# Kernel tuning notes

Hardware: AMD Instinct MI355X
Metric: run time of the kernel (lower is better)

The kernel has to match this reference:

```python
import jax, jax.numpy as jnp
import numpy as np

CHANNELS, STYLE_DIM, N_HEADS, N_TOK = 512, 256, 2, 50
HEAD_DIM = STYLE_DIM // N_HEADS
SCALE = STYLE_DIM ** (-0.5)


def setup_inputs() -> dict:
    key = jax.random.key(0)
    ks = jax.random.split(key, 12)
    B, T = 16, 4096
    s = lambda fan_in: 1.0 / np.sqrt(fan_in)
    return {
        "x": jax.random.normal(ks[0], (B, CHANNELS, T), jnp.float32),
        "style": jax.random.normal(ks[1], (B, N_TOK, STYLE_DIM), jnp.float32),
        "key_emb": jax.random.normal(ks[2], (1, N_TOK, STYLE_DIM), jnp.float32) * 0.3,
        "Wq": jax.random.uniform(ks[3], (STYLE_DIM, CHANNELS), jnp.float32, -s(CHANNELS), s(CHANNELS)),
        "bq": jax.random.uniform(ks[4], (STYLE_DIM,), jnp.float32, -s(CHANNELS), s(CHANNELS)),
        "Wk": jax.random.uniform(ks[5], (STYLE_DIM, STYLE_DIM), jnp.float32, -s(STYLE_DIM), s(STYLE_DIM)),
        "bk": jax.random.uniform(ks[6], (STYLE_DIM,), jnp.float32, -s(STYLE_DIM), s(STYLE_DIM)),
        "Wv": jax.random.uniform(ks[7], (STYLE_DIM, STYLE_DIM), jnp.float32, -s(STYLE_DIM), s(STYLE_DIM)),
        "bv": jax.random.uniform(ks[8], (STYLE_DIM,), jnp.float32, -s(STYLE_DIM), s(STYLE_DIM)),
        "Wo": jax.random.uniform(ks[9], (CHANNELS, STYLE_DIM), jnp.float32, -s(STYLE_DIM), s(STYLE_DIM)),
        "bo": jax.random.uniform(ks[10], (CHANNELS,), jnp.float32, -s(STYLE_DIM), s(STYLE_DIM)),
    }


def reference(x, style, key_emb, Wq, bq, Wk, bk, Wv, bv, Wo, bo):
    B, C, T = x.shape
    N = style.shape[1]
    # Q from x (transposed to [B,T,C]); K from static learned embedding; V from style
    q = jnp.einsum('bct,dc->btd', x, Wq) + bq                 # [B,T,style_dim]
    k = jnp.einsum('bns,ds->bnd', jnp.broadcast_to(key_emb, (B, N_TOK, STYLE_DIM)), Wk) + bk
    v = jnp.einsum('bns,ds->bnd', style, Wv) + bv
    # split heads: [B,H,T,hd] / [B,H,N,hd]
    q = q.reshape(B, T, N_HEADS, HEAD_DIM).transpose(0, 2, 1, 3)
    k = k.reshape(B, N_TOK, N_HEADS, HEAD_DIM).transpose(0, 2, 1, 3)
    v = v.reshape(B, N, N_HEADS, HEAD_DIM).transpose(0, 2, 1, 3)
    # tanh applied to transposed keys before QK^T
    attn = jnp.einsum('bhtd,bhnd->bhtn', q, jnp.tanh(k)) * SCALE
    attn = jax.nn.softmax(attn, axis=-1)
    out = jnp.einsum('bhtn,bhnd->bhtd', attn, v)              # [B,H,T,hd]
    out = out.transpose(0, 2, 1, 3).reshape(B, T, STYLE_DIM)
    out = jnp.einsum('btd,cd->btc', out, Wo) + bo             # [B,T,C]
    return x + out.transpose(0, 2, 1)
```

## Files before the change

### kernel.cpp

```cpp
#include <hip/hip_runtime.h>
#include <stdint.h>

#define CHN 512
#define TDIM 4096
#define SD 256
#define HD 128
#define NTOK 50
#define NP 64
#define NB 16
#define TT 128
#define QPITCH 264
#define XPITCH 132
#define SCALE_ 0.0625f

typedef float f32x4 __attribute__((ext_vector_type(4)));
typedef unsigned int u32x4 __attribute__((ext_vector_type(4)));
typedef short s16x8 __attribute__((ext_vector_type(8)));

__device__ __forceinline__ uint16_t f2bf(float f) {
  union { float f; uint32_t u; } v; v.f = f;
  uint32_t r = (v.u + 0x7fffu + ((v.u >> 16) & 1u)) >> 16;
  return (uint16_t)r;
}
__device__ __forceinline__ uint32_t packbf(float lo, float hi) {
  return (uint32_t)f2bf(lo) | ((uint32_t)f2bf(hi) << 16);
}
__device__ __forceinline__ void mfma_bf16(f32x4& d, u32x4 a, u32x4 b) {
  union { u32x4 u; s16x8 s; } ua, ub;
  ua.u = a; ub.u = b;
  d = __builtin_amdgcn_mfma_f32_16x16x32_bf16(ua.s, ub.s, d, 0, 0, 0);
}

__global__ void conv_w_kernel(const float* __restrict__ Wq, const float* __restrict__ Wo,
                              uint16_t* __restrict__ wqb, uint16_t* __restrict__ wob) {
  int i = blockIdx.x * 256 + threadIdx.x;
  wqb[i] = f2bf(Wq[i]);
  wob[i] = f2bf(Wo[i]);
}

__global__ void prep_kv_kernel(const float* __restrict__ style, const float* __restrict__ kemb,
                               const float* __restrict__ Wk, const float* __restrict__ bk,
                               const float* __restrict__ Wv, const float* __restrict__ bv,
                               uint16_t* __restrict__ kt, uint16_t* __restrict__ vT) {
  int id = blockIdx.x * 256 + threadIdx.x;
  if (id < 2 * NP * HD) {
    int dh = id & (HD - 1);
    int n  = (id >> 7) & (NP - 1);
    int h  = id >> 13;
    uint16_t r = 0;
    if (n < NTOK) {
      int d = h * HD + dh;
      float acc = bk[d];
      const float* er = kemb + (size_t)n * SD;
      const float* wr = Wk + (size_t)d * SD;
      for (int s = 0; s < SD; s += 4) {
        float4 e = *(const float4*)(er + s);
        float4 w4 = *(const float4*)(wr + s);
        acc += e.x * w4.x + e.y * w4.y + e.z * w4.z + e.w * w4.w;
      }
      r = f2bf(tanhf(acc));
    }
    kt[id] = r;
  } else {
    int vid = id - 2 * NP * HD;
    int n  = vid & (NP - 1);
    int dh = (vid >> 6) & (HD - 1);
    int h  = (vid >> 13) & 1;
    int bb = vid >> 14;
    uint16_t r = 0;
    if (n < NTOK) {
      int d = h * HD + dh;
      float acc = bv[d];
      const float* sr = style + (size_t)(bb * NTOK + n) * SD;
      const float* wr = Wv + (size_t)d * SD;
      for (int s = 0; s < SD; s += 4) {
        float4 e = *(const float4*)(sr + s);
        float4 w4 = *(const float4*)(wr + s);
        acc += e.x * w4.x + e.y * w4.y + e.z * w4.z + e.w * w4.w;
      }
      r = f2bf(acc);
    }
    vT[vid] = r;
  }
}

__global__ __launch_bounds__(512, 2) void fused_kernel(
    const float* __restrict__ x, const float* __restrict__ bq, const float* __restrict__ bo,
    const uint16_t* __restrict__ wqb, const uint16_t* __restrict__ wob,
    const uint16_t* __restrict__ kt, const uint16_t* __restrict__ vT,
    float* __restrict__ out) {
  __shared__ uint16_t qs[TT * QPITCH];

  const int bb = blockIdx.y;
  const int t0 = blockIdx.x * TT;
  const int tid = threadIdx.x;
  const int lane = tid & 63;
  const int w = tid >> 6;
  const int l15 = lane & 15;
  const int g = lane >> 4;
  const int wm = w >> 1;
  const int wn = w & 1;

  const float* xb = x + (size_t)bb * CHN * TDIM + t0;

  f32x4 acc[4][4];
#pragma unroll
  for (int mt = 0; mt < 4; ++mt)
#pragma unroll
    for (int nt = 0; nt < 4; ++nt) acc[mt][nt] = (f32x4){0.f, 0.f, 0.f, 0.f};

  const int ts = tid & (TT - 1);
  const int cp0 = tid >> 7;

  for (int cc = 0; cc < 4; ++cc) {
    const int c0 = cc * 128;
    if (cc) __syncthreads();
#pragma unroll
    for (int p = 0; p < 16; ++p) {
      int cl = 2 * cp0 + 8 * p;
      float a0 = xb[(size_t)(c0 + cl) * TDIM + ts];
      float a1 = xb[(size_t)(c0 + cl + 1) * TDIM + ts];
      *(uint32_t*)&qs[ts * XPITCH + cl] = packbf(a0, a1);
    }
    __syncthreads();
#pragma unroll
    for (int ks = 0; ks < 4; ++ks) {
      u32x4 afr[4];
#pragma unroll
      for (int mt = 0; mt < 4; ++mt) {
        int dr = (wm * 4 + mt) * 16 + l15;
        afr[mt] = *(const u32x4*)(wqb + (size_t)dr * CHN + c0 + ks * 32 + g * 8);
      }
#pragma unroll
      for (int nt = 0; nt < 4; ++nt) {
        int tr = (wn * 4 + nt) * 16 + l15;
        const uint16_t* pb = &qs[tr * XPITCH + ks * 32 + g * 8];
        uint2 lo = *(const uint2*)pb;
        uint2 hi = *(const uint2*)(pb + 4);
        u32x4 bfr = (u32x4){lo.x, lo.y, hi.x, hi.y};
#pragma unroll
        for (int mt = 0; mt < 4; ++mt) mfma_bf16(acc[mt][nt], afr[mt], bfr);
      }
    }
  }
  __syncthreads();
#pragma unroll
  for (int mt = 0; mt < 4; ++mt) {
    int d0 = (wm * 4 + mt) * 16 + g * 4;
    float4 bqv = *(const float4*)(bq + d0);
#pragma unroll
    for (int nt = 0; nt < 4; ++nt) {
      int tr = (wn * 4 + nt) * 16 + l15;
      uint2 wv;
      wv.x = packbf(acc[mt][nt][0] + bqv.x, acc[mt][nt][1] + bqv.y);
      wv.y = packbf(acc[mt][nt][2] + bqv.z, acc[mt][nt][3] + bqv.w);
      *(uint2*)&qs[tr * QPITCH + d0] = wv;
    }
  }
  __syncthreads();

  const int tmy = w * 16 + l15;
  const uint16_t* qrow = &qs[tmy * QPITCH];
  const int l1 = l15 + 16 * ((2 * g) & 3);
  const int l2 = l15 + 16 * ((2 * g + 1) & 3);
  const bool hiH = (g >> 1) != 0;

#pragma unroll
  for (int h = 0; h < 2; ++h) {
    u32x4 bq4[4];
#pragma unroll
    for (int ks = 0; ks < 4; ++ks)
      bq4[ks] = *(const u32x4*)(qrow + h * HD + ks * 32 + g * 8);

    f32x4 sac[4];
#pragma unroll
    for (int mtn = 0; mtn < 4; ++mtn) {
      sac[mtn] = (f32x4){0.f, 0.f, 0.f, 0.f};
#pragma unroll
      for (int ks = 0; ks < 4; ++ks) {
        u32x4 afr = *(const u32x4*)(kt + (size_t)(h * NP + mtn * 16 + l15) * HD + ks * 32 + g * 8);
        mfma_bf16(sac[mtn], afr, bq4[ks]);
      }
    }
    float pv[4][4];
    float mx = -3.0e38f;
#pragma unroll
    for (int mtn = 0; mtn < 4; ++mtn)
#pragma unroll
      for (int j = 0; j < 4; ++j) {
        int n = mtn * 16 + g * 4 + j;
        float s = (n < NTOK) ? sac[mtn][j] * SCALE_ : -3.0e38f;
        pv[mtn][j] = s;
        mx = fmaxf(mx, s);
      }
    mx = fmaxf(mx, __shfl_xor(mx, 16, 64));
    mx = fmaxf(mx, __shfl_xor(mx, 32, 64));
    float sum = 0.f;
#pragma unroll
    for (int mtn = 0; mtn < 4; ++mtn)
#pragma unroll
      for (int j = 0; j < 4; ++j) {
        float e = __expf(pv[mtn][j] - mx);
        pv[mtn][j] = e;
        sum += e;
      }
    sum += __shfl_xor(sum, 16, 64);
    sum += __shfl_xor(sum, 32, 64);
    float inv = 1.0f / sum;
    uint32_t pk[4][2];
#pragma unroll
    for (int mtn = 0; mtn < 4; ++mtn) {
      pk[mtn][0] = packbf(pv[mtn][0] * inv, pv[mtn][1] * inv);
      pk[mtn][1] = packbf(pv[mtn][2] * inv, pv[mtn][3] * inv);
    }
    u32x4 bp[2];
#pragma unroll
    for (int ks = 0; ks < 2; ++ks) {
      uint32_t a0 = (uint32_t)__shfl((int)pk[2 * ks][0], l1, 64);
      uint32_t b0 = (uint32_t)__shfl((int)pk[2 * ks + 1][0], l1, 64);
      uint32_t a1 = (uint32_t)__shfl((int)pk[2 * ks][1], l1, 64);
      uint32_t b1 = (uint32_t)__shfl((int)pk[2 * ks + 1][1], l1, 64);
      uint32_t a2 = (uint32_t)__shfl((int)pk[2 * ks][0], l2, 64);
      uint32_t b2 = (uint32_t)__shfl((int)pk[2 * ks + 1][0], l2, 64);
      uint32_t a3 = (uint32_t)__shfl((int)pk[2 * ks][1], l2, 64);
      uint32_t b3 = (uint32_t)__shfl((int)pk[2 * ks + 1][1], l2, 64);
      bp[ks] = (u32x4){hiH ? b0 : a0, hiH ? b1 : a1, hiH ? b2 : a2, hiH ? b3 : a3};
    }
    const uint16_t* vb = vT + (size_t)((bb * 2 + h) * HD) * NP;
#pragma unroll
    for (int mtd = 0; mtd < 8; ++mtd) {
      f32x4 oac = (f32x4){0.f, 0.f, 0.f, 0.f};
#pragma unroll
      for (int ks = 0; ks < 2; ++ks) {
        u32x4 afr = *(const u32x4*)(vb + (size_t)(mtd * 16 + l15) * NP + ks * 32 + g * 8);
        mfma_bf16(oac, afr, bp[ks]);
      }
      int d0 = h * HD + mtd * 16 + g * 4;
      uint2 wv;
      wv.x = packbf(oac[0], oac[1]);
      wv.y = packbf(oac[2], oac[3]);
      *(uint2*)&qs[tmy * QPITCH + d0] = wv;
    }
  }

  u32x4 ak[8];
#pragma unroll
  for (int ks = 0; ks < 8; ++ks)
    ak[ks] = *(const u32x4*)(qrow + ks * 32 + g * 8);

  const float* xr = x + (size_t)bb * CHN * TDIM;
  float* orow = out + (size_t)bb * CHN * TDIM;
  const int t4 = t0 + w * 16 + g * 4;
#pragma unroll 2
  for (int nt = 0; nt < 32; ++nt) {
    int c = nt * 16 + l15;
    const uint16_t* wrow = wob + (size_t)c * SD;
    f32x4 yac = (f32x4){0.f, 0.f, 0.f, 0.f};
#pragma unroll
    for (int ks = 0; ks < 8; ++ks) {
      u32x4 bfr = *(const u32x4*)(wrow + ks * 32 + g * 8);
      mfma_bf16(yac, ak[ks], bfr);
    }
    float bov = bo[c];
    float4 xv = *(const float4*)(xr + (size_t)c * TDIM + t4);
    float4 ov;
    ov.x = xv.x + yac[0] + bov;
    ov.y = xv.y + yac[1] + bov;
    ov.z = xv.z + yac[2] + bov;
    ov.w = xv.w + yac[3] + bov;
    *(float4*)(orow + (size_t)c * TDIM + t4) = ov;
  }
}

extern "C" void kernel_launch(void* const* d_in, const int* in_sizes, int n_in,
                              void* d_out, int out_size, void* d_ws, size_t ws_size,
                              hipStream_t stream) {
  const float* x     = (const float*)d_in[0];
  const float* style = (const float*)d_in[1];
  const float* kemb  = (const float*)d_in[2];
  const float* Wq    = (const float*)d_in[3];
  const float* bq    = (const float*)d_in[4];
  const float* Wk    = (const float*)d_in[5];
  const float* bk    = (const float*)d_in[6];
  const float* Wv    = (const float*)d_in[7];
  const float* bv    = (const float*)d_in[8];
  const float* Wo    = (const float*)d_in[9];
  const float* bo    = (const float*)d_in[10];
  float* out = (float*)d_out;

  uint16_t* wqb = (uint16_t*)d_ws;
  uint16_t* wob = wqb + 131072;
  uint16_t* ktw = wob + 131072;
  uint16_t* vTw = ktw + 16384;

  conv_w_kernel<<<512, 256, 0, stream>>>(Wq, Wo, wqb, wob);
  prep_kv_kernel<<<1088, 256, 0, stream>>>(style, kemb, Wk, bk, Wv, bv, ktw, vTw);
  dim3 grid(TDIM / TT, NB);
  fused_kernel<<<grid, 512, 0, stream>>>(x, bq, bo, wqb, wob, ktw, vTw, out);
}
```

Measured before the change: 264.2 us.

## Prefetch x tiles into registers for Q projection and residual epilogue

The Q-projection staging loop now loads x with float2 vector loads into registers and prefetches the next 128-channel chunk while the current chunk is consumed, so global latency overlaps the MFMA work. The output epilogue keeps an 8-deep register ring of residual x float4 loads issued ahead of use, and that loop is now fully unrolled. This aims to hide global memory latency but raises register pressure, which may reduce occupancy. Each thread now writes two LDS rows per pair, changing the bank-access pattern.

After: 265.8 us. Within noise of the previous version (+0.6%).

```diff
diff --git a/kernel.cpp b/kernel.cpp
--- a/kernel.cpp
+++ b/kernel.cpp
@@ -109,18 +109,35 @@
 #pragma unroll
     for (int nt = 0; nt < 4; ++nt) acc[mt][nt] = (f32x4){0.f, 0.f, 0.f, 0.f};
 
-  const int ts = tid & (TT - 1);
-  const int cp0 = tid >> 7;
+  const int ts2 = (lane << 1) | 0;
+  const int tse = ((tid & 63) << 1);
+  const int cb  = (tid >> 6) << 1;
+
+  float2 va[8], vb[8];
+#pragma unroll
+  for (int p = 0; p < 8; ++p) {
+    int c = cb + 16 * p;
+    va[p] = *(const float2*)(xb + (size_t)c * TDIM + tse);
+    vb[p] = *(const float2*)(xb + (size_t)(c + 1) * TDIM + tse);
+  }
 
   for (int cc = 0; cc < 4; ++cc) {
     const int c0 = cc * 128;
-    if (cc) __syncthreads();
-#pragma unroll
-    for (int p = 0; p < 16; ++p) {
-      int cl = 2 * cp0 + 8 * p;
-      float a0 = xb[(size_t)(c0 + cl) * TDIM + ts];
-      float a1 = xb[(size_t)(c0 + cl + 1) * TDIM + ts];
-      *(uint32_t*)&qs[ts * XPITCH + cl] = packbf(a0, a1);
+    __syncthreads();
+#pragma unroll
+    for (int p = 0; p < 8; ++p) {
+      int cl = cb + 16 * p;
+      *(uint32_t*)&qs[tse * XPITCH + cl]       = packbf(va[p].x, vb[p].x);
+      *(uint32_t*)&qs[(tse + 1) * XPITCH + cl] = packbf(va[p].y, vb[p].y);
+    }
+    if (cc < 3) {
+      const int c0n = c0 + 128;
+#pragma unroll
+      for (int p = 0; p < 8; ++p) {
+        int c = c0n + cb + 16 * p;
+        va[p] = *(const float2*)(xb + (size_t)c * TDIM + tse);
+        vb[p] = *(const float2*)(xb + (size_t)(c + 1) * TDIM + tse);
+      }
     }
     __syncthreads();
 #pragma unroll
@@ -226,13 +243,13 @@
       uint32_t b3 = (uint32_t)__shfl((int)pk[2 * ks + 1][1], l2, 64);
       bp[ks] = (u32x4){hiH ? b0 : a0, hiH ? b1 : a1, hiH ? b2 : a2, hiH ? b3 : a3};
     }
-    const uint16_t* vb = vT + (size_t)((bb * 2 + h) * HD) * NP;
+    const uint16_t* vb2 = vT + (size_t)((bb * 2 + h) * HD) * NP;
 #pragma unroll
     for (int mtd = 0; mtd < 8; ++mtd) {
       f32x4 oac = (f32x4){0.f, 0.f, 0.f, 0.f};
 #pragma unroll
       for (int ks = 0; ks < 2; ++ks) {
-        u32x4 afr = *(const u32x4*)(vb + (size_t)(mtd * 16 + l15) * NP + ks * 32 + g * 8);
+        u32x4 afr = *(const u32x4*)(vb2 + (size_t)(mtd * 16 + l15) * NP + ks * 32 + g * 8);
         mfma_bf16(oac, afr, bp[ks]);
       }
       int d0 = h * HD + mtd * 16 + g * 4;
@@ -251,7 +268,14 @@
   const float* xr = x + (size_t)bb * CHN * TDIM;
   float* orow = out + (size_t)bb * CHN * TDIM;
   const int t4 = t0 + w * 16 + g * 4;
-#pragma unroll 2
+
+  float4 xg[8];
+#pragma unroll
+  for (int i = 0; i < 8; ++i) {
+    int c = i * 16 + l15;
+    xg[i] = *(const float4*)(xr + (size_t)c * TDIM + t4);
+  }
+#pragma unroll
   for (int nt = 0; nt < 32; ++nt) {
     int c = nt * 16 + l15;
     const uint16_t* wrow = wob + (size_t)c * SD;
@@ -262,7 +286,11 @@
       mfma_bf16(yac, ak[ks], bfr);
     }
     float bov = bo[c];
-    float4 xv = *(const float4*)(xr + (size_t)c * TDIM + t4);
+    float4 xv = xg[nt & 7];
+    if (nt + 8 < 32) {
+      int c2 = (nt + 8) * 16 + l15;
+      xg[nt & 7] = *(const float4*)(xr + (size_t)c2 * TDIM + t4);
+    }
     float4 ov;
     ov.x = xv.x + yac[0] + bov;
     ov.y = xv.y + yac[1] + bov;
```
